# Kernel tuning notes

Hardware: AMD Instinct MI355X
Metric: run time of the kernel (lower is better)

## Reference

```python
import jax, jax.numpy as jnp
import numpy as np

N_ITER = 15
ITER_LR = 0.1


def setup_inputs() -> dict:
    key = jax.random.key(0)
    ks = jax.random.split(key, 4)
    dims = [784, 512, 256, 10]
    x = jax.random.normal(ks[0], (32768, dims[0]), dtype=jnp.float32)
    # weights[i]: (dims[i+1], dims[i]) scaled by sqrt(2/dims[i+1]); biases[i]: (dims[i],) zeros
    W0 = jax.random.normal(ks[1], (dims[1], dims[0]), dtype=jnp.float32) * np.sqrt(2.0 / dims[1]).astype(np.float32)
    W1 = jax.random.normal(ks[2], (dims[2], dims[1]), dtype=jnp.float32) * np.sqrt(2.0 / dims[2]).astype(np.float32)
    W2 = jax.random.normal(ks[3], (dims[3], dims[2]), dtype=jnp.float32) * np.sqrt(2.0 / dims[3]).astype(np.float32)
    b0 = jnp.zeros((dims[0],), dtype=jnp.float32)
    b1 = jnp.zeros((dims[1],), dtype=jnp.float32)
    b2 = jnp.zeros((dims[2],), dtype=jnp.float32)
    return {"x": x, "W0": W0, "W1": W1, "W2": W2, "b0": b0, "b1": b1, "b2": b2}


def reference(x, W0, W1, W2, b0, b1, b2):
    # feedforward pass: mus[i+1] = relu(mus[i] @ W[i].T)
    m1 = jax.nn.relu(x @ W0.T)    # [B, 512]
    m2 = jax.nn.relu(m1 @ W1.T)   # [B, 256]
    m3 = jax.nn.relu(m2 @ W2.T)   # [B, 10]

    # iterative predictive-coding updates: for l in {1, 2}:
    #   pred = relu(mus[l+1] @ W[l] + b[l]); mus[l] = relu(mus[l] - iter_lr * (mus[l] - pred))
    def body(_, carry):
        m1, m2, m3 = carry
        pred1 = jax.nn.relu(m2 @ W1 + b1)                 # uses m2 before its update (loop order)
        m1 = jax.nn.relu(m1 - ITER_LR * (m1 - pred1))
        pred2 = jax.nn.relu(m3 @ W2 + b2)
        m2 = jax.nn.relu(m2 - ITER_LR * (m2 - pred2))
        return (m1, m2, m3)

    m1, m2, m3 = jax.lax.fori_loop(0, N_ITER, body, (m1, m2, m3))
    # mus[-1] is never updated by the loop; returned as-is (faithful to the torch code)
    return m3
```

## Files before the change

kernel.cpp:

```cpp
#include <hip/hip_runtime.h>

typedef __bf16 bhalf;
typedef bhalf bhalf8 __attribute__((ext_vector_type(8)));
typedef float f32x4 __attribute__((ext_vector_type(4)));
typedef unsigned short u16;
typedef u16 u16x8 __attribute__((ext_vector_type(8)));

__device__ __forceinline__ u16 f2bf(float f) {
  union { float f; unsigned u; } v; v.f = f;
  unsigned r = v.u + 0x7FFFu + ((v.u >> 16) & 1u);
  return (u16)(r >> 16);
}

__device__ __forceinline__ int swz(int L)  { return L ^ (((L >> 7) & 7) << 4); }
__device__ __forceinline__ int swzM(int L) { return L ^ ((((L >> 10) ^ (L >> 13)) & 7) << 4); }

#define GLL16(gp, lp) __builtin_amdgcn_global_load_lds( \
    (const __attribute__((address_space(1))) unsigned int*)(gp), \
    (__attribute__((address_space(3))) unsigned int*)(lp), 16, 0, 0)

#define SB() __builtin_amdgcn_sched_barrier(0)

#define KP0 832
#define W0E (512 * KP0)
#define W1E (256 * 512)
#define W2E (16 * 256)

__global__ __launch_bounds__(256) void cvt_weights(
    const float* __restrict__ W0, const float* __restrict__ W1,
    const float* __restrict__ W2,
    u16* __restrict__ W0b, u16* __restrict__ W1b, u16* __restrict__ W2b)
{
  int i = blockIdx.x * 256 + threadIdx.x;
  if (i < W0E) {
    int r = i / KP0, k = i - r * KP0;
    W0b[i] = (k < 784) ? f2bf(W0[r * 784 + k]) : (u16)0;
    return;
  }
  i -= W0E;
  if (i < W1E) { W1b[i] = f2bf(W1[i]); return; }
  i -= W1E;
  if (i < W2E) {
    int r = i >> 8, c = i & 255;
    W2b[i] = (r < 10) ? f2bf(W2[r * 256 + c]) : (u16)0;
  }
}

__global__ __launch_bounds__(512) void fused3(
    const float* __restrict__ x, const u16* __restrict__ Wb,
    const u16* __restrict__ W1b, const u16* __restrict__ W2b,
    float* __restrict__ out)
{
  extern __shared__ u16 ldsu[];
  char* lds = (char*)ldsu;
  const int t = threadIdx.x, w = t >> 6, lane = t & 63;
  const size_t rbase = (size_t)blockIdx.x * 128;
  const int wr = w >> 2, wc = w & 3, fr = lane & 15, fg = lane >> 4;

  int aO[4];
#pragma unroll
  for (int m = 0; m < 4; ++m) aO[m] = swz((wr * 64 + m * 16 + fr) * 128 + fg * 16);
  int bO[4];
#pragma unroll
  for (int j = 0; j < 4; ++j) bO[j] = swz((wc * 128 + j * 16 + fr) * 64 + fg * 16);

  const u16* bSrcP[4];
#pragma unroll
  for (int i = 0; i < 4; ++i) {
    int P = (w * 4 + i) * 1024 + lane * 16;
    int U = swz(P);
    bSrcP[i] = Wb + (size_t)(U >> 6) * KP0 + ((U & 63) >> 1);
  }
  const float* xRow[2]; int aKc[2];
#pragma unroll
  for (int c2 = 0; c2 < 2; ++c2) {
    int P = c2 * 8192 + t * 16;
    int U = swz(P);
    xRow[c2] = x + (rbase + (U >> 7)) * (size_t)784;
    aKc[c2] = (U & 127) >> 1;
  }

  f32x4 acc[4][8];
#pragma unroll
  for (int m = 0; m < 4; ++m)
#pragma unroll
    for (int n = 0; n < 8; ++n) acc[m][n] = (f32x4){0.f, 0.f, 0.f, 0.f};

  bhalf8 afA[4], bf[4];
  f32x4 xrE[2][2], xrO[2][2];

  auto loadX = [&](int tt2, f32x4 (&xr)[2][2]) {
#pragma unroll
    for (int c2 = 0; c2 < 2; ++c2) {
      int k = tt2 * 64 + aKc[c2];
      const float* p = xRow[c2] + ((k < 784) ? k : 0);
      xr[c2][0] = *(const f32x4*)p; xr[c2][1] = *(const f32x4*)(p + 4);
    }
  };
  auto cvtW = [&](int aB, f32x4 (&xr)[2][2]) {
#pragma unroll
    for (int c2 = 0; c2 < 2; ++c2) {
      u16x8 v;
#pragma unroll
      for (int j = 0; j < 4; ++j) { v[j] = f2bf(xr[c2][0][j]); v[4 + j] = f2bf(xr[c2][1][j]); }
      *(u16x8*)(lds + aB + c2 * 8192 + t * 16) = v;
    }
  };
  auto gllLo = [&](int H) {
    char* bb = lds + 32768 + (H % 3) * 32768;
    GLL16(bSrcP[0] + H * 32, bb + (w * 4 + 0) * 1024);
    GLL16(bSrcP[1] + H * 32, bb + (w * 4 + 1) * 1024);
  };
  auto gllHi = [&](int H) {
    char* bb = lds + 32768 + (H % 3) * 32768;
    GLL16(bSrcP[2] + H * 32, bb + (w * 4 + 2) * 1024);
    GLL16(bSrcP[3] + H * 32, bb + (w * 4 + 3) * 1024);
  };
  auto rdA = [&](int aB, int ks) {
#pragma unroll
    for (int m = 0; m < 4; ++m)
      afA[m] = *(const bhalf8*)(lds + aB + (aO[m] ^ (ks << 6)));
  };
  auto rdBq = [&](int H, int hi) {
    const char* bb = lds + 32768 + (H % 3) * 32768 + hi * 4096;
#pragma unroll
    for (int j = 0; j < 4; ++j) bf[j] = *(const bhalf8*)(bb + bO[j]);
  };
  auto mfmaLoQ = [&]() {
    __builtin_amdgcn_s_setprio(1);
#pragma unroll
    for (int m = 0; m < 4; ++m)
#pragma unroll
      for (int n = 0; n < 4; ++n)
        acc[m][n] = __builtin_amdgcn_mfma_f32_16x16x32_bf16(afA[m], bf[n], acc[m][n], 0, 0, 0);
    __builtin_amdgcn_s_setprio(0);
  };
  auto mfmaHiQ = [&]() {
    __builtin_amdgcn_s_setprio(1);
#pragma unroll
    for (int m = 0; m < 4; ++m)
#pragma unroll
      for (int n = 0; n < 4; ++n)
        acc[m][4 + n] = __builtin_amdgcn_mfma_f32_16x16x32_bf16(afA[m], bf[n], acc[m][4 + n], 0, 0, 0);
    __builtin_amdgcn_s_setprio(0);
  };

  auto tile = [&](int tt, f32x4 (&xrLd)[2][2], f32x4 (&xrCv)[2][2],
                  bool doStage, bool doX, int vmPh4, bool vm0Ph2) {
    const int aB = (tt & 1) * 16384;
    const int H0 = 2 * tt, H1 = 2 * tt + 1;
    rdA(aB, 0); rdBq(H0, 0);
    if (doStage) gllLo(H0 + 2);
    __builtin_amdgcn_s_barrier();
    asm volatile("s_waitcnt lgkmcnt(0)" ::: "memory"); SB();
    mfmaLoQ();
    __builtin_amdgcn_s_barrier();
    rdBq(H0, 1);
    if (doStage) gllHi(H0 + 2);
    __builtin_amdgcn_s_barrier();
    asm volatile("s_waitcnt lgkmcnt(0)" ::: "memory"); SB();
    mfmaHiQ();
    if (vm0Ph2) { asm volatile("s_waitcnt vmcnt(0)" ::: "memory"); }
    else        { asm volatile("s_waitcnt vmcnt(4)" ::: "memory"); }
    __builtin_amdgcn_s_barrier();
    rdA(aB, 1); rdBq(H1, 0);
    if (doStage) gllLo(H1 + 2);
    if (doX) loadX(tt + 2, xrLd);
    __builtin_amdgcn_s_barrier();
    asm volatile("s_waitcnt lgkmcnt(0)" ::: "memory"); SB();
    mfmaLoQ();
    __builtin_amdgcn_s_barrier();
    rdBq(H1, 1);
    if (tt < 12) cvtW(aB ^ 16384, xrCv);
    if (doStage) gllHi(H1 + 2);
    __builtin_amdgcn_s_barrier();
    asm volatile("s_waitcnt lgkmcnt(0)" ::: "memory"); SB();
    mfmaHiQ();
    if (vmPh4 == 8)      { asm volatile("s_waitcnt vmcnt(8)" ::: "memory"); }
    else if (vmPh4 == 4) { asm volatile("s_waitcnt vmcnt(4)" ::: "memory"); }
    __builtin_amdgcn_s_barrier();
  };

  gllLo(0); gllHi(0);
  gllLo(1); gllHi(1);
  loadX(0, xrE);
  loadX(1, xrO);
  cvtW(0, xrE);
  asm volatile("s_waitcnt lgkmcnt(0)" ::: "memory");
  __builtin_amdgcn_s_barrier();

  for (int i = 0; i < 5; ++i) {
    tile(2 * i,     xrE, xrO, true, true, 8, false);
    tile(2 * i + 1, xrO, xrE, true, true, 8, false);
  }
  tile(10, xrE, xrO, true,  true,  8, false);
  tile(11, xrO, xrE, true,  false, 4, false);
  tile(12, xrE, xrO, false, false, -1, true);

  const u16* w1Src[2];
#pragma unroll
  for (int i = 0; i < 2; ++i) {
    int P = (w * 2 + i) * 1024 + lane * 16;
    int U = swz(P);
    w1Src[i] = W1b + (size_t)(U >> 6) * 512 + ((U & 63) >> 1);
  }
#pragma unroll
  for (int i = 0; i < 2; ++i) GLL16(w1Src[i], lds + 131072 + (w * 2 + i) * 1024);

#pragma unroll
  for (int m = 0; m < 4; ++m)
#pragma unroll
    for (int n = 0; n < 8; ++n)
#pragma unroll
      for (int q = 0; q < 4; ++q) {
        int row = wr * 64 + m * 16 + fg * 4 + q;
        int col = wc * 128 + n * 16 + fr;
        float vv = acc[m][n][q];
        vv = vv > 0.f ? vv : 0.f;
        *(u16*)(lds + swzM(row * 1024 + col * 2)) = f2bf(vv);
      }
  __syncthreads();

  int a2O[4], b2O[4];
#pragma unroll
  for (int m = 0; m < 4; ++m) a2O[m] = (wr * 64 + m * 16 + fr) * 1024 + fg * 16;
#pragma unroll
  for (int n = 0; n < 4; ++n) b2O[n] = (wc * 64 + n * 16 + fr) * 64 + fg * 16;

  f32x4 acc2[4][4];
#pragma unroll
  for (int m = 0; m < 4; ++m)
#pragma unroll
    for (int n = 0; n < 4; ++n) acc2[m][n] = (f32x4){0.f, 0.f, 0.f, 0.f};

  for (int kt = 0; kt < 16; ++kt) {
    const char* wbuf = lds + 131072 + (kt & 1) * 16384;
    asm volatile("s_waitcnt vmcnt(0)" ::: "memory");
    __syncthreads();
    if (kt < 15) {
#pragma unroll
      for (int i = 0; i < 2; ++i)
        GLL16(w1Src[i] + (kt + 1) * 32,
              lds + 131072 + ((kt + 1) & 1) * 16384 + (w * 2 + i) * 1024);
    }
    bhalf8 a2[4], b2[4];
#pragma unroll
    for (int m = 0; m < 4; ++m)
      a2[m] = *(const bhalf8*)(lds + swzM(a2O[m] + kt * 64));
#pragma unroll
    for (int n = 0; n < 4; ++n)
      b2[n] = *(const bhalf8*)(wbuf + swz(b2O[n]));
    __builtin_amdgcn_s_setprio(1);
#pragma unroll
    for (int m = 0; m < 4; ++m)
#pragma unroll
      for (int n = 0; n < 4; ++n)
        acc2[m][n] = __builtin_amdgcn_mfma_f32_16x16x32_bf16(a2[m], b2[n], acc2[m][n], 0, 0, 0);
    __builtin_amdgcn_s_setprio(0);
  }
  __syncthreads();

  u16* m2s = (u16*)lds;
  u16* W2s = (u16*)(lds + 67584);
  {
    int r = t >> 5, kc = (t & 31) * 8;
    *(int4*)&W2s[r * 264 + kc] = *(const int4*)(W2b + r * 256 + kc);
  }
#pragma unroll
  for (int m = 0; m < 4; ++m)
#pragma unroll
    for (int n = 0; n < 4; ++n)
#pragma unroll
      for (int q = 0; q < 4; ++q) {
        int row = wr * 64 + m * 16 + fg * 4 + q;
        int col = wc * 64 + n * 16 + fr;
        float vv = acc2[m][n][q];
        vv = vv > 0.f ? vv : 0.f;
        m2s[row * 264 + col] = f2bf(vv);
      }
  __syncthreads();

  {
    f32x4 acc3 = (f32x4){0.f, 0.f, 0.f, 0.f};
    const int arow = w * 16 + fr;
#pragma unroll
    for (int ks = 0; ks < 8; ++ks) {
      bhalf8 a = *(const bhalf8*)&m2s[arow * 264 + ks * 32 + fg * 8];
      bhalf8 b = *(const bhalf8*)&W2s[fr * 264 + ks * 32 + fg * 8];
      acc3 = __builtin_amdgcn_mfma_f32_16x16x32_bf16(a, b, acc3, 0, 0, 0);
    }
    if (fr < 10) {
#pragma unroll
      for (int q = 0; q < 4; ++q) {
        size_t row = rbase + w * 16 + fg * 4 + q;
        float vv = acc3[q];
        out[row * 10 + fr] = vv > 0.f ? vv : 0.f;
      }
    }
  }
}

extern "C" void kernel_launch(void* const* d_in, const int* in_sizes, int n_in,
                              void* d_out, int out_size, void* d_ws, size_t ws_size,
                              hipStream_t stream) {
  const float* x  = (const float*)d_in[0];
  const float* W0 = (const float*)d_in[1];
  const float* W1 = (const float*)d_in[2];
  const float* W2 = (const float*)d_in[3];
  float* out = (float*)d_out;

  char* ws = (char*)d_ws;
  u16* W0b = (u16*)(ws);
  u16* W1b = (u16*)(ws + 851968);
  u16* W2b = (u16*)(ws + 1114112);

  hipFuncSetAttribute((const void*)fused3,
                      hipFuncAttributeMaxDynamicSharedMemorySize, 163840);

  cvt_weights<<<dim3((W0E + W1E + W2E + 255) / 256), dim3(256), 0, stream>>>(
      W0, W1, W2, W0b, W1b, W2b);

  fused3<<<dim3(256), dim3(512), 163840, stream>>>(x, W0b, W1b, W2b, out);
}
```

Before: 53.97 us.

## Shrink layer-0 K tile to 32 and pad K to 800

The first-layer GEMM now uses a K step of 32 instead of 64, so K is padded only to 800 instead of 832 and the 25 stages avoid computing on zero padding. The main loop is restructured into 25 single-stage tiles that each read and convert one x chunk, with fewer barriers per stage but more stages overall. The A buffer and LDS offsets shrink, and the vmcnt waits are retuned. In exchange each stage does fewer MFMAs between barriers, which may expose latency.

```diff
diff --git a/kernel.cpp b/kernel.cpp
--- a/kernel.cpp
+++ b/kernel.cpp
@@ -21,7 +21,7 @@
 
 #define SB() __builtin_amdgcn_sched_barrier(0)
 
-#define KP0 832
+#define KP0 800
 #define W0E (512 * KP0)
 #define W1E (256 * 512)
 #define W2E (16 * 256)
@@ -57,12 +57,11 @@
   const size_t rbase = (size_t)blockIdx.x * 128;
   const int wr = w >> 2, wc = w & 3, fr = lane & 15, fg = lane >> 4;
 
-  int aO[4];
-#pragma unroll
-  for (int m = 0; m < 4; ++m) aO[m] = swz((wr * 64 + m * 16 + fr) * 128 + fg * 16);
-  int bO[4];
-#pragma unroll
-  for (int j = 0; j < 4; ++j) bO[j] = swz((wc * 128 + j * 16 + fr) * 64 + fg * 16);
+  int aO[4], bO[8];
+#pragma unroll
+  for (int m = 0; m < 4; ++m) aO[m] = swz((wr * 64 + m * 16 + fr) * 64 + fg * 16);
+#pragma unroll
+  for (int n = 0; n < 8; ++n) bO[n] = swz((wc * 128 + n * 16 + fr) * 64 + fg * 16);
 
   const u16* bSrcP[4];
 #pragma unroll
@@ -71,13 +70,12 @@
     int U = swz(P);
     bSrcP[i] = Wb + (size_t)(U >> 6) * KP0 + ((U & 63) >> 1);
   }
-  const float* xRow[2]; int aKc[2];
-#pragma unroll
-  for (int c2 = 0; c2 < 2; ++c2) {
-    int P = c2 * 8192 + t * 16;
+  const float* xRow; int aKe;
+  {
+    int P = t * 16;
     int U = swz(P);
-    xRow[c2] = x + (rbase + (U >> 7)) * (size_t)784;
-    aKc[c2] = (U & 127) >> 1;
+    xRow = x + (rbase + (U >> 6)) * (size_t)784;
+    aKe = (U & 63) >> 1;
   }
 
   f32x4 acc[4][8];
@@ -87,46 +85,28 @@
     for (int n = 0; n < 8; ++n) acc[m][n] = (f32x4){0.f, 0.f, 0.f, 0.f};
 
   bhalf8 afA[4], bf[4];
-  f32x4 xrE[2][2], xrO[2][2];
-
-  auto loadX = [&](int tt2, f32x4 (&xr)[2][2]) {
-#pragma unroll
-    for (int c2 = 0; c2 < 2; ++c2) {
-      int k = tt2 * 64 + aKc[c2];
-      const float* p = xRow[c2] + ((k < 784) ? k : 0);
-      xr[c2][0] = *(const f32x4*)p; xr[c2][1] = *(const f32x4*)(p + 4);
-    }
-  };
-  auto cvtW = [&](int aB, f32x4 (&xr)[2][2]) {
-#pragma unroll
-    for (int c2 = 0; c2 < 2; ++c2) {
-      u16x8 v;
-#pragma unroll
-      for (int j = 0; j < 4; ++j) { v[j] = f2bf(xr[c2][0][j]); v[4 + j] = f2bf(xr[c2][1][j]); }
-      *(u16x8*)(lds + aB + c2 * 8192 + t * 16) = v;
-    }
-  };
-  auto gllLo = [&](int H) {
-    char* bb = lds + 32768 + (H % 3) * 32768;
-    GLL16(bSrcP[0] + H * 32, bb + (w * 4 + 0) * 1024);
-    GLL16(bSrcP[1] + H * 32, bb + (w * 4 + 1) * 1024);
-  };
-  auto gllHi = [&](int H) {
-    char* bb = lds + 32768 + (H % 3) * 32768;
-    GLL16(bSrcP[2] + H * 32, bb + (w * 4 + 2) * 1024);
-    GLL16(bSrcP[3] + H * 32, bb + (w * 4 + 3) * 1024);
-  };
-  auto rdA = [&](int aB, int ks) {
-#pragma unroll
-    for (int m = 0; m < 4; ++m)
-      afA[m] = *(const bhalf8*)(lds + aB + (aO[m] ^ (ks << 6)));
-  };
-  auto rdBq = [&](int H, int hi) {
-    const char* bb = lds + 32768 + (H % 3) * 32768 + hi * 4096;
-#pragma unroll
-    for (int j = 0; j < 4; ++j) bf[j] = *(const bhalf8*)(bb + bO[j]);
-  };
-  auto mfmaLoQ = [&]() {
+  f32x4 xrE[2], xrO[2];
+
+  auto loadX = [&](int s, f32x4 (&xr)[2]) {
+    int k = s * 32 + aKe;
+    const float* p = xRow + ((k < 784) ? k : 0);
+    xr[0] = *(const f32x4*)p; xr[1] = *(const f32x4*)(p + 4);
+  };
+  auto cvtW = [&](int aB, f32x4 (&xr)[2]) {
+    u16x8 v;
+#pragma unroll
+    for (int j = 0; j < 4; ++j) { v[j] = f2bf(xr[0][j]); v[4 + j] = f2bf(xr[1][j]); }
+    *(u16x8*)(lds + aB + t * 16) = v;
+  };
+  auto rdA = [&](int aB) {
+#pragma unroll
+    for (int m = 0; m < 4; ++m) afA[m] = *(const bhalf8*)(lds + aB + aO[m]);
+  };
+  auto rdBq = [&](const char* bb, int hi) {
+#pragma unroll
+    for (int j = 0; j < 4; ++j) bf[j] = *(const bhalf8*)(bb + bO[hi * 4 + j]);
+  };
+  auto mfmaLo = [&]() {
     __builtin_amdgcn_s_setprio(1);
 #pragma unroll
     for (int m = 0; m < 4; ++m)
@@ -135,7 +115,7 @@
         acc[m][n] = __builtin_amdgcn_mfma_f32_16x16x32_bf16(afA[m], bf[n], acc[m][n], 0, 0, 0);
     __builtin_amdgcn_s_setprio(0);
   };
-  auto mfmaHiQ = [&]() {
+  auto mfmaHi = [&]() {
     __builtin_amdgcn_s_setprio(1);
 #pragma unroll
     for (int m = 0; m < 4; ++m)
@@ -145,57 +125,53 @@
     __builtin_amdgcn_s_setprio(0);
   };
 
-  auto tile = [&](int tt, f32x4 (&xrLd)[2][2], f32x4 (&xrCv)[2][2],
-                  bool doStage, bool doX, int vmPh4, bool vm0Ph2) {
-    const int aB = (tt & 1) * 16384;
-    const int H0 = 2 * tt, H1 = 2 * tt + 1;
-    rdA(aB, 0); rdBq(H0, 0);
-    if (doStage) gllLo(H0 + 2);
+  auto tile = [&](int tt, f32x4 (&xLd)[2], f32x4 (&xCv)[2],
+                  bool doStage, bool doX, bool doCvt, int vmEnd) {
+    const int aB = (tt & 1) * 8192;
+    const char* bbCur = lds + 16384 + (tt % 3) * 32768;
+    char* bbNxt = lds + 16384 + ((tt + 2) % 3) * 32768;
+    rdA(aB); rdBq(bbCur, 0);
+    if (doStage) {
+      GLL16(bSrcP[0] + (tt + 2) * 32, bbNxt + (w * 4 + 0) * 1024);
+      GLL16(bSrcP[1] + (tt + 2) * 32, bbNxt + (w * 4 + 1) * 1024);
+    }
+    if (doX) loadX(tt + 2, xLd);
     __builtin_amdgcn_s_barrier();
     asm volatile("s_waitcnt lgkmcnt(0)" ::: "memory"); SB();
-    mfmaLoQ();
+    mfmaLo();
     __builtin_amdgcn_s_barrier();
-    rdBq(H0, 1);
-    if (doStage) gllHi(H0 + 2);
+    rdBq(bbCur, 1);
+    if (doCvt) cvtW(aB ^ 8192, xCv);
+    if (doStage) {
+      GLL16(bSrcP[2] + (tt + 2) * 32, bbNxt + (w * 4 + 2) * 1024);
+      GLL16(bSrcP[3] + (tt + 2) * 32, bbNxt + (w * 4 + 3) * 1024);
+    }
     __builtin_amdgcn_s_barrier();
     asm volatile("s_waitcnt lgkmcnt(0)" ::: "memory"); SB();
-    mfmaHiQ();
-    if (vm0Ph2) { asm volatile("s_waitcnt vmcnt(0)" ::: "memory"); }
-    else        { asm volatile("s_waitcnt vmcnt(4)" ::: "memory"); }
+    mfmaHi();
+    if (vmEnd == 6)      { asm volatile("s_waitcnt vmcnt(6)" ::: "memory"); }
+    else if (vmEnd == 0) { asm volatile("s_waitcnt vmcnt(0)" ::: "memory"); }
     __builtin_amdgcn_s_barrier();
-    rdA(aB, 1); rdBq(H1, 0);
-    if (doStage) gllLo(H1 + 2);
-    if (doX) loadX(tt + 2, xrLd);
-    __builtin_amdgcn_s_barrier();
-    asm volatile("s_waitcnt lgkmcnt(0)" ::: "memory"); SB();
-    mfmaLoQ();
-    __builtin_amdgcn_s_barrier();
-    rdBq(H1, 1);
-    if (tt < 12) cvtW(aB ^ 16384, xrCv);
-    if (doStage) gllHi(H1 + 2);
-    __builtin_amdgcn_s_barrier();
-    asm volatile("s_waitcnt lgkmcnt(0)" ::: "memory"); SB();
-    mfmaHiQ();
-    if (vmPh4 == 8)      { asm volatile("s_waitcnt vmcnt(8)" ::: "memory"); }
-    else if (vmPh4 == 4) { asm volatile("s_waitcnt vmcnt(4)" ::: "memory"); }
-    __builtin_amdgcn_s_barrier();
-  };
-
-  gllLo(0); gllHi(0);
-  gllLo(1); gllHi(1);
+  };
+
+#pragma unroll
+  for (int i = 0; i < 4; ++i) GLL16(bSrcP[i], lds + 16384 + (w * 4 + i) * 1024);
   loadX(0, xrE);
+#pragma unroll
+  for (int i = 0; i < 4; ++i) GLL16(bSrcP[i] + 32, lds + 16384 + 32768 + (w * 4 + i) * 1024);
   loadX(1, xrO);
   cvtW(0, xrE);
   asm volatile("s_waitcnt lgkmcnt(0)" ::: "memory");
   __builtin_amdgcn_s_barrier();
 
-  for (int i = 0; i < 5; ++i) {
-    tile(2 * i,     xrE, xrO, true, true, 8, false);
-    tile(2 * i + 1, xrO, xrE, true, true, 8, false);
-  }
-  tile(10, xrE, xrO, true,  true,  8, false);
-  tile(11, xrO, xrE, true,  false, 4, false);
-  tile(12, xrE, xrO, false, false, -1, true);
+  for (int i = 0; i < 11; ++i) {
+    tile(2 * i,     xrE, xrO, true, true, true, 6);
+    tile(2 * i + 1, xrO, xrE, true, true, true, 6);
+  }
+  tile(22, xrE, xrO, true,  true,  true,  6);
+  tile(23, xrO, xrE, false, false, true,  0);
+  tile(24, xrE, xrO, false, false, false, -1);
+  __builtin_amdgcn_s_barrier();
 
   const u16* w1Src[2];
 #pragma unroll
@@ -311,8 +287,8 @@
 
   char* ws = (char*)d_ws;
   u16* W0b = (u16*)(ws);
-  u16* W1b = (u16*)(ws + 851968);
-  u16* W2b = (u16*)(ws + 1114112);
+  u16* W1b = (u16*)(ws + 819200);
+  u16* W2b = (u16*)(ws + 1081344);
 
   hipFuncSetAttribute((const void*)fused3,
                       hipFuncAttributeMaxDynamicSharedMemorySize, 163840);
```

Result: no change. 54.90 us (+1.7%).

## Trim layer-0 K padding to 800 and restructure the tail tile schedule

Applied to the files above, without the earlier changes.

Reduces the padded K dimension of W0 from 832 to 800, dropping one K-tile (a half tile) of layer-0 MFMA work and weight staging. The final tile becomes a single half-step with no staging. The conversion of x to bf16 moves after the second MFMA batch, with waits merged into the closing waitcnt. In the layer-1 loop, the A-fragment LDS reads are hoisted ahead of the barrier and the weight prefetch. The risk is that the pipeline's vmcnt bookkeeping and buffer parity become wrong in the shortened tail.

```diff
diff --git a/kernel.cpp b/kernel.cpp
--- a/kernel.cpp
+++ b/kernel.cpp
@@ -21,7 +21,7 @@
 
 #define SB() __builtin_amdgcn_sched_barrier(0)
 
-#define KP0 832
+#define KP0 800
 #define W0E (512 * KP0)
 #define W1E (256 * 512)
 #define W2E (16 * 256)
@@ -146,38 +146,37 @@
   };
 
   auto tile = [&](int tt, f32x4 (&xrLd)[2][2], f32x4 (&xrCv)[2][2],
-                  bool doStage, bool doX, int vmPh4, bool vm0Ph2) {
+                  bool stageA, bool stageB, bool doX, bool doCvt, int vmPh4) {
     const int aB = (tt & 1) * 16384;
     const int H0 = 2 * tt, H1 = 2 * tt + 1;
     rdA(aB, 0); rdBq(H0, 0);
-    if (doStage) gllLo(H0 + 2);
+    if (stageA) gllLo(H0 + 2);
     __builtin_amdgcn_s_barrier();
     asm volatile("s_waitcnt lgkmcnt(0)" ::: "memory"); SB();
     mfmaLoQ();
     __builtin_amdgcn_s_barrier();
     rdBq(H0, 1);
-    if (doStage) gllHi(H0 + 2);
+    if (stageA) gllHi(H0 + 2);
     __builtin_amdgcn_s_barrier();
     asm volatile("s_waitcnt lgkmcnt(0)" ::: "memory"); SB();
     mfmaHiQ();
-    if (vm0Ph2) { asm volatile("s_waitcnt vmcnt(0)" ::: "memory"); }
-    else        { asm volatile("s_waitcnt vmcnt(4)" ::: "memory"); }
+    asm volatile("s_waitcnt vmcnt(4)" ::: "memory");
     __builtin_amdgcn_s_barrier();
     rdA(aB, 1); rdBq(H1, 0);
-    if (doStage) gllLo(H1 + 2);
+    if (stageB) gllLo(H1 + 2);
     if (doX) loadX(tt + 2, xrLd);
     __builtin_amdgcn_s_barrier();
     asm volatile("s_waitcnt lgkmcnt(0)" ::: "memory"); SB();
     mfmaLoQ();
     __builtin_amdgcn_s_barrier();
     rdBq(H1, 1);
-    if (tt < 12) cvtW(aB ^ 16384, xrCv);
-    if (doStage) gllHi(H1 + 2);
+    if (stageB) gllHi(H1 + 2);
     __builtin_amdgcn_s_barrier();
     asm volatile("s_waitcnt lgkmcnt(0)" ::: "memory"); SB();
     mfmaHiQ();
-    if (vmPh4 == 8)      { asm volatile("s_waitcnt vmcnt(8)" ::: "memory"); }
-    else if (vmPh4 == 4) { asm volatile("s_waitcnt vmcnt(4)" ::: "memory"); }
+    if (doCvt) cvtW(aB ^ 16384, xrCv);
+    if (vmPh4 == 8) { asm volatile("s_waitcnt vmcnt(8) lgkmcnt(0)" ::: "memory"); }
+    else            { asm volatile("s_waitcnt vmcnt(0) lgkmcnt(0)" ::: "memory"); }
     __builtin_amdgcn_s_barrier();
   };
 
@@ -190,12 +189,22 @@
   __builtin_amdgcn_s_barrier();
 
   for (int i = 0; i < 5; ++i) {
-    tile(2 * i,     xrE, xrO, true, true, 8, false);
-    tile(2 * i + 1, xrO, xrE, true, true, 8, false);
-  }
-  tile(10, xrE, xrO, true,  true,  8, false);
-  tile(11, xrO, xrE, true,  false, 4, false);
-  tile(12, xrE, xrO, false, false, -1, true);
+    tile(2 * i,     xrE, xrO, true, true, true, true, 8);
+    tile(2 * i + 1, xrO, xrE, true, true, true, true, 8);
+  }
+  tile(10, xrE, xrO, true, true,  true,  true, 8);
+  tile(11, xrO, xrE, true, false, false, true, 0);
+  {
+    rdA(0, 0); rdBq(24, 0);
+    __builtin_amdgcn_s_barrier();
+    asm volatile("s_waitcnt lgkmcnt(0)" ::: "memory"); SB();
+    mfmaLoQ();
+    __builtin_amdgcn_s_barrier();
+    rdBq(24, 1);
+    asm volatile("s_waitcnt lgkmcnt(0)" ::: "memory"); SB();
+    mfmaHiQ();
+    __builtin_amdgcn_s_barrier();
+  }
 
   const u16* w1Src[2];
 #pragma unroll
@@ -235,6 +244,10 @@
 
   for (int kt = 0; kt < 16; ++kt) {
     const char* wbuf = lds + 131072 + (kt & 1) * 16384;
+    bhalf8 a2[4], b2[4];
+#pragma unroll
+    for (int m = 0; m < 4; ++m)
+      a2[m] = *(const bhalf8*)(lds + swzM(a2O[m] + kt * 64));
     asm volatile("s_waitcnt vmcnt(0)" ::: "memory");
     __syncthreads();
     if (kt < 15) {
@@ -243,10 +256,6 @@
         GLL16(w1Src[i] + (kt + 1) * 32,
               lds + 131072 + ((kt + 1) & 1) * 16384 + (w * 2 + i) * 1024);
     }
-    bhalf8 a2[4], b2[4];
-#pragma unroll
-    for (int m = 0; m < 4; ++m)
-      a2[m] = *(const bhalf8*)(lds + swzM(a2O[m] + kt * 64));
 #pragma unroll
     for (int n = 0; n < 4; ++n)
       b2[n] = *(const bhalf8*)(wbuf + swz(b2O[n]));
@@ -311,8 +320,8 @@
 
   char* ws = (char*)d_ws;
   u16* W0b = (u16*)(ws);
-  u16* W1b = (u16*)(ws + 851968);
-  u16* W2b = (u16*)(ws + 1114112);
+  u16* W1b = (u16*)(ws + 819200);
+  u16* W2b = (u16*)(ws + 1081344);
 
   hipFuncSetAttribute((const void*)fused3,
                       hipFuncAttributeMaxDynamicSharedMemorySize, 163840);
```

Result: no change. 54.34 us (+0.7%).
